# Performance work log

Hardware: AMD Instinct MI355X
Metric: run time of the kernel (lower is better)

The kernel has to match this reference:

```python
import jax, jax.numpy as jnp
import numpy as np

T, B, D, U = 256, 128, 1024, 1024

def _orthogonal(key, shape, gain=1.0, dtype=jnp.float32):
    # Orthogonal init matching tf.initializers.Orthogonal
    n_rows, n_cols = shape
    big = max(n_rows, n_cols)
    a = jax.random.normal(key, (big, min(n_rows, n_cols)), dtype=jnp.float32)
    q, r = jnp.linalg.qr(a)
    q = q * jnp.sign(jnp.diag(r))
    q = q[:n_rows, :n_cols] if n_rows >= n_cols else q.T[:n_rows, :n_cols]
    return (gain * q).astype(dtype)

def setup_inputs() -> dict:
    key = jax.random.key(0)
    k1, k2, k3, k4 = jax.random.split(key, 4)
    inputs = jax.random.normal(k1, (T, B, D), dtype=jnp.float32)
    states = jnp.zeros((2, B, U), dtype=jnp.float32)  # stacked (c, h)
    masks = jax.random.randint(k2, (T, B), 0, 2).astype(jnp.int32)
    kernelx = _orthogonal(k3, (D, 4 * U), gain=1.0)
    kernelh = _orthogonal(k4, (U, 4 * U), gain=1.0)
    bias = jnp.zeros((4 * U,), dtype=jnp.float32)
    return {"inputs": inputs, "states": states, "masks": masks,
            "kernelx": kernelx, "kernelh": kernelh, "bias": bias}

def reference(inputs, states, masks, kernelx, kernelh, bias):
    c0, h0 = states[0], states[1]
    # mask semantics from source: m = 1 - masks; state is zeroed where mask==1
    m = (1.0 - masks.astype(inputs.dtype))[..., None]       # [T, B, 1]
    # Precompute input contribution for all steps (one big GEMM)
    xz = jnp.einsum('tbd,dk->tbk', inputs, kernelx) + bias  # [T, B, 4U]

    def step(carry, xs):
        c, h = carry
        xz_t, m_t = xs
        c = c * m_t
        h = h * m_t
        z = xz_t + h @ kernelh                              # [B, 4U]
        i, f, o, u = jnp.split(z, 4, axis=-1)
        i = jax.nn.sigmoid(i)
        f = jax.nn.sigmoid(f)
        o = jax.nn.sigmoid(o)
        u = jnp.tanh(u)
        c = f * c + i * u
        h = o * jnp.tanh(c)
        return (c, h), h

    (c, h), out = jax.lax.scan(step, (c0, h0), (xz, m))
    return out, jnp.stack([c, h])
```

## Files before the change

### kernel.cpp

```cpp
#include <hip/hip_runtime.h>


typedef float  f32x4 __attribute__((ext_vector_type(4)));
typedef float  f32x2 __attribute__((ext_vector_type(2)));
typedef __bf16 bf16x8 __attribute__((ext_vector_type(8)));
typedef unsigned short us8 __attribute__((ext_vector_type(8)));
typedef unsigned short us4 __attribute__((ext_vector_type(4)));
typedef unsigned int   u32x4 __attribute__((ext_vector_type(4)));

#define TT 256
#define BB 128
#define DD 1024
#define UU 1024
#define NZ 4096

typedef __attribute__((address_space(3))) unsigned       lds_u32;
typedef const __attribute__((address_space(1))) unsigned glob_u32;

__device__ __forceinline__ unsigned short f2bf(float x) {
  union { float f; unsigned u; } v; v.f = x;
  unsigned r = v.u + 0x7fffu + ((v.u >> 16) & 1u);
  return (unsigned short)(r >> 16);
}
__device__ __forceinline__ float bf2f(unsigned short b) {
  union { unsigned u; float f; } v; v.u = ((unsigned)b) << 16;
  return v.f;
}
__device__ __forceinline__ float sigm(float x) { return 1.f / (1.f + __expf(-x)); }
__device__ __forceinline__ float tanh_(float x) { return 1.f - 2.f / (__expf(2.f * x) + 1.f); }

__global__ __launch_bounds__(256) void k_prep(const float* __restrict__ inputs,
                                              unsigned short* __restrict__ Abf,
                                              const float* __restrict__ kernelx,
                                              unsigned short* __restrict__ WxT,
                                              const float* __restrict__ kernelh,
                                              unsigned short* __restrict__ WhT,
                                              unsigned* __restrict__ flags) {
  __shared__ unsigned short tile[64][72];
  const int b = blockIdx.x;
  const int t = threadIdx.x;

  if (b == 0) {
    flags[t] = 0;
    flags[t + 256] = 0;
  }

  if (b < 16384) {
    const int i = b * 256 + t;
    const float4 a = *(const float4*)(inputs + (size_t)i * 8);
    const float4 c = *(const float4*)(inputs + (size_t)i * 8 + 4);
    us8 v;
    v[0] = f2bf(a.x); v[1] = f2bf(a.y); v[2] = f2bf(a.z); v[3] = f2bf(a.w);
    v[4] = f2bf(c.x); v[5] = f2bf(c.y); v[6] = f2bf(c.z); v[7] = f2bf(c.w);
    *(us8*)(Abf + (size_t)i * 8) = v;
    return;
  }

  const float* in          = (b < 17408) ? kernelx : kernelh;
  unsigned short* outp     = (b < 17408) ? WxT : WhT;
  const int bb = (b - 16384) & 1023;
  const int ni = bb & 63;
  const int ki = bb >> 6;
  const int c = t & 63, r0 = t >> 6;
#pragma unroll
  for (int rr = 0; rr < 16; ++rr) {
    int r = r0 * 16 + rr;
    tile[r][c] = f2bf(in[(size_t)(ki * 64 + r) * NZ + ni * 64 + c]);
  }
  __syncthreads();
  const int kcol = t & 63, ng = t >> 6;
#pragma unroll
  for (int cc = 0; cc < 16; ++cc) {
    int n_off = ng * 16 + cc;
    outp[(size_t)(ni * 64 + n_off) * DD + ki * 64 + kcol] = tile[kcol][n_off];
  }
}

__global__ __launch_bounds__(256, 2) void k_gemm_bf(const unsigned short* __restrict__ A,
                                                    const unsigned short* __restrict__ Bt,
                                                    unsigned short* __restrict__ C) {
  __shared__ unsigned short Al[2][128 * 64];
  __shared__ unsigned short Bl[2][128 * 64];
  const int bx = blockIdx.x;
  const int wgid = (bx & 7) * 1024 + (bx >> 3);
  const int tm = wgid >> 5, tn = wgid & 31;
  const int tid = threadIdx.x;
  const int wave = tid >> 6, lane = tid & 63;
  const int wr = wave >> 1, wc = wave & 1;
  const int l15 = lane & 15, kg = lane >> 4;

  f32x4 acc[4][4] = {};

  const int srow = tid >> 3;
  const int scol = (tid & 7) * 8;
  const unsigned sdst = tid * 8;

  auto stage = [&](int buf, int kt) {
#pragma unroll
    for (int i = 0; i < 4; ++i) {
      __builtin_amdgcn_global_load_lds(
          (glob_u32*)(A  + (size_t)(tm * 128 + i * 32 + srow) * DD + kt * 64 + scol),
          (lds_u32*)&Al[buf][i * 2048 + sdst], 16, 0, 0);
      __builtin_amdgcn_global_load_lds(
          (glob_u32*)(Bt + (size_t)(tn * 128 + i * 32 + srow) * DD + kt * 64 + scol),
          (lds_u32*)&Bl[buf][i * 2048 + sdst], 16, 0, 0);
    }
  };

  stage(0, 0);
  __syncthreads();

  for (int kt = 0; kt < 16; ++kt) {
    const int buf = kt & 1;
    if (kt < 15) stage(buf ^ 1, kt + 1);
#pragma unroll
    for (int ks = 0; ks < 2; ++ks) {
      bf16x8 af[4], bfr[4];
#pragma unroll
      for (int mi = 0; mi < 4; ++mi)
        af[mi] = *(const bf16x8*)&Al[buf][(wr * 64 + mi * 16 + l15) * 64 + ks * 32 + kg * 8];
#pragma unroll
      for (int ni = 0; ni < 4; ++ni)
        bfr[ni] = *(const bf16x8*)&Bl[buf][(wc * 64 + ni * 16 + l15) * 64 + ks * 32 + kg * 8];
#pragma unroll
      for (int mi = 0; mi < 4; ++mi)
#pragma unroll
        for (int ni = 0; ni < 4; ++ni)
          acc[ni][mi] = __builtin_amdgcn_mfma_f32_16x16x32_bf16(bfr[ni], af[mi], acc[ni][mi], 0, 0, 0);
    }
    __syncthreads();
  }

#pragma unroll
  for (int mi = 0; mi < 4; ++mi) {
    const size_t row = (size_t)tm * 128 + wr * 64 + mi * 16 + l15;
#pragma unroll
    for (int ni = 0; ni < 4; ++ni) {
      const size_t col = (size_t)tn * 128 + wc * 64 + ni * 16 + kg * 4;
      us4 v;
      v[0] = f2bf(acc[ni][mi][0]); v[1] = f2bf(acc[ni][mi][1]);
      v[2] = f2bf(acc[ni][mi][2]); v[3] = f2bf(acc[ni][mi][3]);
      *(us4*)(C + row * NZ + col) = v;
    }
  }
}

#define SCAN_QUARTER(Q, VMSTR)                                                  \
  {                                                                             \
    asm volatile("s_waitcnt " VMSTR ::: "memory");                              \
    __builtin_amdgcn_sched_barrier(0);                                          \
    *(u32x4*)(hlds_c + sbase + (Q) * 512)         = sv[(Q) * 2];                \
    *(u32x4*)(hlds_c + sbase + 16384 + (Q) * 512) = sv[(Q) * 2 + 1];            \
    asm volatile("s_waitcnt lgkmcnt(0)" ::: "memory");                          \
    __builtin_amdgcn_sched_barrier(0);                                          \
    __builtin_amdgcn_s_barrier();                                               \
    _Pragma("unroll")                                                           \
    for (int ks = (Q) * 8; ks < (Q) * 8 + 8; ++ks) {                            \
      const char* p = ((ks & 1) ? hp1 : hp0) + (ks >> 1) * 128;                 \
      bf16x8 a = *(const bf16x8*)p;                                             \
      acc0 = __builtin_amdgcn_mfma_f32_16x16x32_bf16(a, __builtin_bit_cast(bf16x8, w0[ks]), acc0, 0, 0, 0); \
      acc1 = __builtin_amdgcn_mfma_f32_16x16x32_bf16(a, __builtin_bit_cast(bf16x8, w1[ks]), acc1, 0, 0, 0); \
    }                                                                           \
  }

__global__ __launch_bounds__(256, 1) void k_scan(const float* __restrict__ init_cs,
                                                 const int* __restrict__ masks,
                                                 const unsigned short* __restrict__ WhT,
                                                 const float* __restrict__ bias,
                                                 const unsigned short* __restrict__ xz,
                                                 float* __restrict__ out,
                                                 unsigned short* __restrict__ hglob,
                                                 unsigned* __restrict__ flags) {
  __shared__ char  hlds_c[32768];
  __shared__ float zlds[4][16][33];
  __shared__ int   mlds[TT * 16 + 16];

  const int tid = threadIdx.x;
  const int wave = tid >> 6, lane = tid & 63;
  const int l15 = lane & 15, kg = lane >> 4;
  const int blk = blockIdx.x;
  const int g = blk & 7;
  const int sb = blk >> 3;
  const int u0 = sb * 32;
  const int row0 = g * 16;
  unsigned* fl = flags + g * 64;

  u32x4 w0[32], w1[32];
  {
    const size_t r0 = (size_t)(wave * UU + u0 + l15) * DD;
    const size_t r1 = (size_t)(wave * UU + u0 + 16 + l15) * DD;
#pragma unroll
    for (int ks = 0; ks < 32; ++ks) {
      w0[ks] = *(const u32x4*)(WhT + r0 + ks * 32 + kg * 8);
      w1[ks] = *(const u32x4*)(WhT + r1 + ks * 32 + kg * 8);
    }
#pragma unroll
    for (int ks = 0; ks < 32; ++ks) {
      asm volatile("" : "+v"(w0[ks]));
      asm volatile("" : "+v"(w1[ks]));
    }
  }

  for (int i = 0; i < 16; ++i) {
    int idx = i * 256 + tid;
    mlds[idx] = masks[(size_t)(idx >> 4) * BB + row0 + (idx & 15)];
  }
  if (tid < 16) mlds[TT * 16 + tid] = 0;

  const int er = tid >> 4;
  const int ec = (tid & 15) * 2;
  const int grow = row0 + er;
  const int guu = u0 + ec;

  float bs0[4], bs1[4];
#pragma unroll
  for (int gt = 0; gt < 4; ++gt) {
    bs0[gt] = bias[gt * UU + guu];
    bs1[gt] = bias[gt * UU + guu + 1];
  }

  float cv0 = init_cs[(size_t)grow * UU + guu];
  float cv1 = init_cs[(size_t)grow * UU + guu + 1];
  float hv0 = init_cs[(size_t)BB * UU + grow * UU + guu];
  float hv1 = init_cs[(size_t)BB * UU + grow * UU + guu + 1];

  const unsigned wswz = ((unsigned)(er & 7)) << 4;
  const unsigned hoff = (unsigned)er * 2048u + ((((unsigned)guu) * 2u) ^ wswz);

  {
    int m0 = masks[grow];
    float s = m0 ? 0.f : 1.f;
    char* base = (char*)hglob + (size_t)g * 32768 + hoff;
    unsigned pv = ((unsigned)f2bf(hv1 * s) << 16) | f2bf(hv0 * s);
    *(unsigned*)base = pv;
  }
  __syncthreads();
  if (tid == 0) fl[sb] = 1;
  if (wave == 0) {
    unsigned v;
    do { v = __hip_atomic_load(&fl[lane & 31], __ATOMIC_RELAXED, __HIP_MEMORY_SCOPE_AGENT); }
    while (!__all(v >= 1));
  }
  __syncthreads();

  const unsigned rswz = ((unsigned)(l15 & 7)) << 4;
  const char* hp0 = hlds_c + l15 * 2048 + (((unsigned)(kg * 16 + 0)) ^ rswz);
  const char* hp1 = hlds_c + l15 * 2048 + (((unsigned)(kg * 16 + 64)) ^ rswz);

  const unsigned sbase = ((unsigned)(tid >> 5)) * 2048u + ((unsigned)(tid & 31)) * 16u;

  for (int t = 0; t < TT; ++t) {
    const char* gsrc = (const char*)hglob + ((size_t)((t & 1) * 8 + g)) * 32768;

    u32x4 sv[8];
#pragma unroll
    for (int q = 0; q < 4; ++q) {
#pragma unroll
      for (int j = 0; j < 2; ++j) {
        const char* ap = gsrc + sbase + j * 16384 + q * 512;
        asm volatile("global_load_dwordx4 %0, %1, off sc0" : "=v"(sv[q * 2 + j]) : "v"(ap));
      }
    }

    f32x4 acc0 = {0.f, 0.f, 0.f, 0.f};
    f32x4 acc1 = {0.f, 0.f, 0.f, 0.f};

    SCAN_QUARTER(0, "vmcnt(6)")
    SCAN_QUARTER(1, "vmcnt(4)")

    unsigned xzv[4];
    {
      const size_t xrow = ((size_t)(t * BB + grow)) * NZ;
#pragma unroll
      for (int gt = 0; gt < 4; ++gt)
        xzv[gt] = *(const unsigned*)(xz + xrow + gt * UU + guu);
    }

    SCAN_QUARTER(2, "vmcnt(6)")
    SCAN_QUARTER(3, "vmcnt(4)")

#pragma unroll
    for (int j = 0; j < 4; ++j) {
      zlds[wave][kg * 4 + j][l15] = acc0[j];
      zlds[wave][kg * 4 + j][16 + l15] = acc1[j];
    }
    __syncthreads();

    const int mcur = mlds[t * 16 + er];
    const int mnxt = mlds[(t + 1) * 16 + er];
    float z0[4], z1[4];
#pragma unroll
    for (int gt = 0; gt < 4; ++gt) {
      z0[gt] = zlds[gt][er][ec]     + bs0[gt] + bf2f((unsigned short)(xzv[gt] & 0xffffu));
      z1[gt] = zlds[gt][er][ec + 1] + bs1[gt] + bf2f((unsigned short)(xzv[gt] >> 16));
    }
    const float sm = mcur ? 0.f : 1.f;
    cv0 *= sm; cv1 *= sm;
    {
      float ig = sigm(z0[0]), fg = sigm(z0[1]), og = sigm(z0[2]), ug = tanh_(z0[3]);
      cv0 = fg * cv0 + ig * ug;
      hv0 = og * tanh_(cv0);
    }
    {
      float ig = sigm(z1[0]), fg = sigm(z1[1]), og = sigm(z1[2]), ug = tanh_(z1[3]);
      cv1 = fg * cv1 + ig * ug;
      hv1 = og * tanh_(cv1);
    }

    {
      const float sn = mnxt ? 0.f : 1.f;
      char* hdst = (char*)hglob + ((size_t)(((t + 1) & 1) * 8 + g)) * 32768 + hoff;
      unsigned pv = ((unsigned)f2bf(hv1 * sn) << 16) | f2bf(hv0 * sn);
      asm volatile("global_store_dword %0, %1, off" :: "v"(hdst), "v"(pv) : "memory");
      float* odst = out + (size_t)t * (BB * UU) + (size_t)grow * UU + guu;
      f32x2 ov = {hv0, hv1};
      asm volatile("global_store_dwordx2 %0, %1, off" :: "v"(odst), "v"(ov) : "memory");
    }
    asm volatile("s_waitcnt vmcnt(1)" ::: "memory");
    __builtin_amdgcn_sched_barrier(0);
    __builtin_amdgcn_s_barrier();
    if (tid == 0) fl[sb] = (unsigned)(t + 2);
    if (wave == 0) {
      const unsigned tgt = (unsigned)(t + 2);
      unsigned v;
      do { v = __hip_atomic_load(&fl[lane & 31], __ATOMIC_RELAXED, __HIP_MEMORY_SCOPE_AGENT); }
      while (!__all(v >= tgt));
    }
    __builtin_amdgcn_s_barrier();
  }

  float* so = out + (size_t)TT * BB * UU;
  *(f32x2*)(so + (size_t)grow * UU + guu) = (f32x2){cv0, cv1};
  *(f32x2*)(so + (size_t)BB * UU + grow * UU + guu) = (f32x2){hv0, hv1};
}

extern "C" void kernel_launch(void* const* d_in, const int* in_sizes, int n_in,
                              void* d_out, int out_size, void* d_ws, size_t ws_size,
                              hipStream_t stream) {
  const float* inputs  = (const float*)d_in[0];
  const float* states  = (const float*)d_in[1];
  const int*   masks   = (const int*)d_in[2];
  const float* kernelx = (const float*)d_in[3];
  const float* kernelh = (const float*)d_in[4];
  const float* bias    = (const float*)d_in[5];
  float* out = (float*)d_out;
  char* ws = (char*)d_ws;

  unsigned* flags       = (unsigned*)ws;
  unsigned short* hglob = (unsigned short*)(ws + 65536);
  unsigned short* WhT   = (unsigned short*)(ws + (size_t)2  * 1048576);
  unsigned short* WxT   = (unsigned short*)(ws + (size_t)10 * 1048576);
  unsigned short* Abf   = (unsigned short*)(ws + (size_t)18 * 1048576);
  unsigned short* xzbig = (unsigned short*)(ws + (size_t)82 * 1048576);

  k_prep<<<dim3(18432), dim3(256), 0, stream>>>(inputs, Abf, kernelx, WxT,
                                                kernelh, WhT, flags);
  k_gemm_bf<<<dim3(8192), dim3(256), 0, stream>>>(Abf, WxT, xzbig);
  k_scan<<<dim3(256), dim3(256), 0, stream>>>(states, masks, WhT, bias, xzbig,
                                              out, hglob, flags);
}
```

Before: 1.201 ms.

## Enlarge input-projection GEMM tiles to 256x256 with swizzled LDS and 8 waves

The bf16 input-projection GEMM moves from 128x128 tiles with 4 waves to 256x256 tiles with 8 waves, each wave computing a 128x64 sub-tile. LDS staging now uses an XOR swizzle on the 16-byte column chunks to avoid bank conflicts on fragment reads. The per-iteration __syncthreads pair is replaced by one explicit vmcnt wait and barrier issued before prefetching the next buffer. This raises arithmetic intensity and cuts global traffic, but doubles LDS use to 128KB and increases register pressure, which may limit occupancy. The GEMM is only one part of a pipeline dominated by the sequential scan.

```diff
diff --git a/kernel.cpp b/kernel.cpp
--- a/kernel.cpp
+++ b/kernel.cpp
@@ -76,70 +76,81 @@
   }
 }
 
-__global__ __launch_bounds__(256, 2) void k_gemm_bf(const unsigned short* __restrict__ A,
+__global__ __launch_bounds__(512, 2) void k_gemm_bf(const unsigned short* __restrict__ A,
                                                     const unsigned short* __restrict__ Bt,
                                                     unsigned short* __restrict__ C) {
-  __shared__ unsigned short Al[2][128 * 64];
-  __shared__ unsigned short Bl[2][128 * 64];
+  __shared__ unsigned short Al[2][16384];
+  __shared__ unsigned short Bl[2][16384];
   const int bx = blockIdx.x;
-  const int wgid = (bx & 7) * 1024 + (bx >> 3);
-  const int tm = wgid >> 5, tn = wgid & 31;
+  const int wgid = (bx & 7) * 256 + (bx >> 3);
+  const int tm = wgid >> 4, tn = wgid & 15;
   const int tid = threadIdx.x;
   const int wave = tid >> 6, lane = tid & 63;
-  const int wr = wave >> 1, wc = wave & 1;
+  const int wr = wave >> 2, wc = wave & 3;
   const int l15 = lane & 15, kg = lane >> 4;
-
-  f32x4 acc[4][4] = {};
+  const int r3 = l15 & 7;
+
+  f32x4 acc[4][8] = {};
 
   const int srow = tid >> 3;
-  const int scol = (tid & 7) * 8;
-  const unsigned sdst = tid * 8;
+  const int sj   = (tid & 7) ^ (srow & 7);
+  const unsigned sdst = (unsigned)tid * 8;
 
   auto stage = [&](int buf, int kt) {
 #pragma unroll
-    for (int i = 0; i < 4; ++i) {
+    for (int i = 0; i < 4; ++i)
       __builtin_amdgcn_global_load_lds(
-          (glob_u32*)(A  + (size_t)(tm * 128 + i * 32 + srow) * DD + kt * 64 + scol),
-          (lds_u32*)&Al[buf][i * 2048 + sdst], 16, 0, 0);
+          (glob_u32*)(A + (size_t)(tm * 256 + i * 64 + srow) * DD + kt * 64 + sj * 8),
+          (lds_u32*)&Al[buf][i * 4096 + sdst], 16, 0, 0);
+#pragma unroll
+    for (int i = 0; i < 4; ++i)
       __builtin_amdgcn_global_load_lds(
-          (glob_u32*)(Bt + (size_t)(tn * 128 + i * 32 + srow) * DD + kt * 64 + scol),
-          (lds_u32*)&Bl[buf][i * 2048 + sdst], 16, 0, 0);
-    }
+          (glob_u32*)(Bt + (size_t)(tn * 256 + i * 64 + srow) * DD + kt * 64 + sj * 8),
+          (lds_u32*)&Bl[buf][i * 4096 + sdst], 16, 0, 0);
   };
 
+  const unsigned aoff0 = ((unsigned)(wr * 128 + l15)) * 128u + ((unsigned)(kg ^ r3)) * 16u;
+  const unsigned aoff1 = ((unsigned)(wr * 128 + l15)) * 128u + ((unsigned)((4 | kg) ^ r3)) * 16u;
+  const unsigned boff0 = ((unsigned)(wc * 64 + l15)) * 128u + ((unsigned)(kg ^ r3)) * 16u;
+  const unsigned boff1 = ((unsigned)(wc * 64 + l15)) * 128u + ((unsigned)((4 | kg) ^ r3)) * 16u;
+
   stage(0, 0);
-  __syncthreads();
 
   for (int kt = 0; kt < 16; ++kt) {
     const int buf = kt & 1;
+    asm volatile("s_waitcnt vmcnt(0)" ::: "memory");
+    __builtin_amdgcn_sched_barrier(0);
+    __builtin_amdgcn_s_barrier();
     if (kt < 15) stage(buf ^ 1, kt + 1);
+
+    const char* Ab = (const char*)&Al[buf][0];
+    const char* Bb = (const char*)&Bl[buf][0];
 #pragma unroll
     for (int ks = 0; ks < 2; ++ks) {
-      bf16x8 af[4], bfr[4];
-#pragma unroll
-      for (int mi = 0; mi < 4; ++mi)
-        af[mi] = *(const bf16x8*)&Al[buf][(wr * 64 + mi * 16 + l15) * 64 + ks * 32 + kg * 8];
-#pragma unroll
-      for (int ni = 0; ni < 4; ++ni)
-        bfr[ni] = *(const bf16x8*)&Bl[buf][(wc * 64 + ni * 16 + l15) * 64 + ks * 32 + kg * 8];
-#pragma unroll
-      for (int mi = 0; mi < 4; ++mi)
-#pragma unroll
-        for (int ni = 0; ni < 4; ++ni)
-          acc[ni][mi] = __builtin_amdgcn_mfma_f32_16x16x32_bf16(bfr[ni], af[mi], acc[ni][mi], 0, 0, 0);
-    }
-    __syncthreads();
-  }
-
-#pragma unroll
-  for (int mi = 0; mi < 4; ++mi) {
-    const size_t row = (size_t)tm * 128 + wr * 64 + mi * 16 + l15;
-#pragma unroll
-    for (int ni = 0; ni < 4; ++ni) {
-      const size_t col = (size_t)tn * 128 + wc * 64 + ni * 16 + kg * 4;
+      const unsigned ao = ks ? aoff1 : aoff0;
+      const unsigned bo = ks ? boff1 : boff0;
+      bf16x8 af[8], bfr[4];
+#pragma unroll
+      for (int mi = 0; mi < 8; ++mi) af[mi] = *(const bf16x8*)(Ab + ao + mi * 2048);
+#pragma unroll
+      for (int nj = 0; nj < 4; ++nj) bfr[nj] = *(const bf16x8*)(Bb + bo + nj * 2048);
+#pragma unroll
+      for (int nj = 0; nj < 4; ++nj)
+#pragma unroll
+        for (int mi = 0; mi < 8; ++mi)
+          acc[nj][mi] = __builtin_amdgcn_mfma_f32_16x16x32_bf16(bfr[nj], af[mi], acc[nj][mi], 0, 0, 0);
+    }
+  }
+
+#pragma unroll
+  for (int mi = 0; mi < 8; ++mi) {
+    const size_t row = (size_t)tm * 256 + wr * 128 + mi * 16 + l15;
+#pragma unroll
+    for (int nj = 0; nj < 4; ++nj) {
+      const size_t col = (size_t)tn * 256 + wc * 64 + nj * 16 + kg * 4;
       us4 v;
-      v[0] = f2bf(acc[ni][mi][0]); v[1] = f2bf(acc[ni][mi][1]);
-      v[2] = f2bf(acc[ni][mi][2]); v[3] = f2bf(acc[ni][mi][3]);
+      v[0] = f2bf(acc[nj][mi][0]); v[1] = f2bf(acc[nj][mi][1]);
+      v[2] = f2bf(acc[nj][mi][2]); v[3] = f2bf(acc[nj][mi][3]);
       *(us4*)(C + row * NZ + col) = v;
     }
   }
@@ -355,7 +366,7 @@
 
   k_prep<<<dim3(18432), dim3(256), 0, stream>>>(inputs, Abf, kernelx, WxT,
                                                 kernelh, WhT, flags);
-  k_gemm_bf<<<dim3(8192), dim3(256), 0, stream>>>(Abf, WxT, xzbig);
+  k_gemm_bf<<<dim3(2048), dim3(512), 0, stream>>>(Abf, WxT, xzbig);
   k_scan<<<dim3(256), dim3(256), 0, stream>>>(states, masks, WhT, bias, xzbig,
                                               out, hglob, flags);
 }
```

Result: faster. 1.087 ms, median of 2 (-9.5%).
